# Optimization experiments

Hardware: AMD Instinct MI355X
Metric: run time of the kernel (lower is better)

## Reference

```python
import jax, jax.numpy as jnp
import numpy as np

N, E, G = 10000, 40000, 128          # nodes, edges, graphs
NF, EF, H, NH, GD, L = 92, 50, 64, 10, 108, 5  # feat dims, hidden, heads, global dim, layers
EPS = 1e-5

def _lrelu(v):
    return jax.nn.leaky_relu(v, 0.2)

def setup_inputs() -> dict:
    key = jax.random.key(0)
    ks = jax.random.split(key, 24)
    def rn(k, shp, s=0.05):
        return jax.random.normal(k, shp, jnp.float32) * s
    return {
        "x": jax.random.normal(ks[0], (N, NF), jnp.float32),
        "edge_index": jax.random.randint(ks[1], (2, E), 0, N, dtype=jnp.int32),
        "edge_attr": jax.random.normal(ks[2], (E, EF), jnp.float32),
        "batch_idx": jnp.sort(jax.random.randint(ks[3], (N,), 0, G, dtype=jnp.int32)),
        "global_features": jax.random.normal(ks[4], (G, GD), jnp.float32),
        "node_W": rn(ks[5], (NF, H)), "node_b": jnp.zeros((H,), jnp.float32),
        "edge_W": rn(ks[6], (EF, H)), "edge_b": jnp.zeros((H,), jnp.float32),
        "conv_W": rn(ks[7], (L, 2 * H, NH * H)),
        "conv_att": rn(ks[8], (L, NH, 2 * H)),
        "conv_b": jnp.zeros((L, H), jnp.float32),
        "conv_gamma": jnp.ones((L, NH), jnp.float32),
        "conv_beta": jnp.zeros((L, NH), jnp.float32),
        "ga_W1": rn(ks[9], (H + GD, H)), "ga_b1": jnp.zeros((H,), jnp.float32),
        "ga_W2": rn(ks[10], (H, 1)), "ga_b2": jnp.zeros((1,), jnp.float32),
        "out_W1": rn(ks[11], (H, H)), "out_b1": jnp.zeros((H,), jnp.float32),
        "out_W2": rn(ks[12], (H, 1)), "out_b2": jnp.zeros((1,), jnp.float32),
    }

def reference(x, edge_index, edge_attr, batch_idx, global_features,
              node_W, node_b, edge_W, edge_b,
              conv_W, conv_att, conv_b, conv_gamma, conv_beta,
              ga_W1, ga_b1, ga_W2, ga_b2, out_W1, out_b1, out_W2, out_b2):
    row, col = edge_index[0], edge_index[1]
    # embeddings
    h = _lrelu(x @ node_W + node_b)            # [N, H]
    ea = _lrelu(edge_attr @ edge_W + edge_b)   # [E, H]
    initial = h
    inv_std = 1.0 / jnp.sqrt(1.0 + EPS)        # DiffGroupNorm eval: running mean=0, var=1
    for i in range(L):
        xi = jnp.concatenate([h[row], ea], axis=-1)               # [E, 2H]
        xj = jnp.concatenate([h[col], ea], axis=-1)
        hi = _lrelu(xi @ conv_W[i]).reshape(E, NH, H)             # [E, NH, H]
        hj = _lrelu(xj @ conv_W[i]).reshape(E, NH, H)
        alpha = jnp.sum(jnp.concatenate([hi, hj], -1) * conv_att[i][None], -1)  # [E, NH]
        alpha = _lrelu(alpha)
        alpha = alpha * inv_std * conv_gamma[i] + conv_beta[i]
        alpha = jax.nn.softmax(alpha, axis=1)                     # softmax over heads
        msg = (hj * alpha[..., None]).reshape(E, NH * H)
        agg = jax.ops.segment_sum(msg, row, num_segments=N).reshape(N, NH, H)
        h_new = agg.mean(axis=1) + conv_b[i]
        h = h + h_new if i > 0 else h_new
    h = h + initial
    # global attention: softmax over nodes within each graph
    g = global_features[batch_idx]                                 # [N, GD]
    s = _lrelu(jnp.concatenate([h, g], -1) @ ga_W1 + ga_b1)
    score = (s @ ga_W2 + ga_b2)[:, 0]                              # [N]
    smax = jax.ops.segment_max(score, batch_idx, num_segments=G)
    ex = jnp.exp(score - smax[batch_idx])
    denom = jax.ops.segment_sum(ex, batch_idx, num_segments=G)
    w = (ex / denom[batch_idx])[:, None]
    h = h * w
    pooled = jax.ops.segment_sum(h, batch_idx, num_segments=G)     # [G, H]
    out = jax.nn.relu(pooled @ out_W1 + out_b1) @ out_W2 + out_b2
    return out[:, 0]
```

## Files before the change

### kernel.cpp

```cpp
#include <hip/hip_runtime.h>

#define LRELU(v) ((v) > 0.f ? (v) : 0.2f * (v))

template <int CTRL, int RMASK>
__device__ __forceinline__ float dpp_add(float v) {
  int moved = __builtin_amdgcn_update_dpp(0, __builtin_bit_cast(int, v), CTRL,
                                          RMASK, 0xf, true);
  return v + __builtin_bit_cast(float, moved);
}
__device__ __forceinline__ float wave_sum(float v) {
  v = dpp_add<0x111, 0xf>(v);
  v = dpp_add<0x112, 0xf>(v);
  v = dpp_add<0x114, 0xf>(v);
  v = dpp_add<0x118, 0xf>(v);
  v = dpp_add<0x142, 0xa>(v);
  v = dpp_add<0x143, 0xc>(v);
  return __builtin_bit_cast(
      float, __builtin_amdgcn_readlane(__builtin_bit_cast(int, v), 63));
}

__global__ __launch_bounds__(256) void embed2_kernel(
    const float* __restrict__ x, const float* __restrict__ nW,
    const float* __restrict__ nb, float* __restrict__ h0, int N_,
    const float* __restrict__ eattr, const float* __restrict__ eW,
    const float* __restrict__ eb, float* __restrict__ ea, int E_,
    int nodeBlocks) {
  const int lane = threadIdx.x & 63;
  const float *X, *W, *b;
  float* out;
  int M, K, r;
  if ((int)blockIdx.x < nodeBlocks) {
    r = blockIdx.x * 4 + (threadIdx.x >> 6);
    X = x; W = nW; b = nb; out = h0; M = N_; K = 92;
  } else {
    r = (blockIdx.x - nodeBlocks) * 4 + (threadIdx.x >> 6);
    X = eattr; W = eW; b = eb; out = ea; M = E_; K = 50;
  }
  r = __builtin_amdgcn_readfirstlane(r);
  if (r >= M) return;
  float acc = b[lane];
  const float* Xr = X + (size_t)r * K;
  const float* Wl = W + lane;
  for (int k = 0; k < K; ++k) acc = fmaf(Xr[k], Wl[(size_t)k * 64], acc);
  acc = LRELU(acc);
  out[(size_t)r * 64 + lane] = acc;
}

__global__ __launch_bounds__(256, 4) void update_gemm_kernel(
    const float* __restrict__ A0, float* __restrict__ h,
    float* __restrict__ agg, const float* __restrict__ bvec,
    const float* __restrict__ W, float* __restrict__ P, int M, int mode) {
  const int lane = threadIdx.x & 63;
  const int wv =
      __builtin_amdgcn_readfirstlane(blockIdx.x * 4 + (threadIdx.x >> 6));
  const int r0 = wv * 4;
  if (r0 >= M) return;
  float hv[4];
  if (mode < 0) {
#pragma unroll
    for (int r = 0; r < 4; ++r) hv[r] = A0[(size_t)(r0 + r) * 64 + lane];
  } else {
    float bl = bvec[lane];
#pragma unroll
    for (int r = 0; r < 4; ++r) {
      size_t idx = (size_t)(r0 + r) * 64 + lane;
      float v = fmaf(agg[idx], 0.1f, bl);
      if (mode >= 1) v += h[idx];
      agg[idx] = 0.f;
      h[idx] = v;
      hv[r] = v;
    }
  }
  float acc[4][10];
#pragma unroll
  for (int r = 0; r < 4; ++r)
#pragma unroll
    for (int q = 0; q < 10; ++q) acc[r][q] = 0.f;
  const float* Wl = W + lane;
  float wa[10], wb[10];
#pragma unroll
  for (int q = 0; q < 10; ++q) wa[q] = Wl[q * 64];
#pragma unroll 1
  for (int k = 0; k < 64; k += 2) {
#pragma unroll
    for (int q = 0; q < 10; ++q) wb[q] = Wl[(k + 1) * 640 + q * 64];
#pragma unroll
    for (int r = 0; r < 4; ++r) {
      float a = __shfl(hv[r], k);
#pragma unroll
      for (int q = 0; q < 10; ++q) acc[r][q] = fmaf(a, wa[q], acc[r][q]);
    }
    if (k + 2 < 64) {
#pragma unroll
      for (int q = 0; q < 10; ++q) wa[q] = Wl[(k + 2) * 640 + q * 64];
    }
#pragma unroll
    for (int r = 0; r < 4; ++r) {
      float a = __shfl(hv[r], k + 1);
#pragma unroll
      for (int q = 0; q < 10; ++q) acc[r][q] = fmaf(a, wb[q], acc[r][q]);
    }
  }
#pragma unroll
  for (int r = 0; r < 4; ++r) {
    float* Crow = P + (size_t)(r0 + r) * 640;
#pragma unroll
    for (int q = 0; q < 10; ++q) Crow[q * 64 + lane] = acc[r][q];
  }
}

__global__ __launch_bounds__(256, 3) void edge_fused_kernel(
    const float* __restrict__ P, const float* __restrict__ ea,
    const float* __restrict__ Wbot,
    const int* __restrict__ row, const int* __restrict__ col,
    const float* __restrict__ att, const float* __restrict__ gamma,
    const float* __restrict__ beta, float* __restrict__ agg, int E_) {
  const int lane = threadIdx.x & 63;
  const int wv =
      __builtin_amdgcn_readfirstlane(blockIdx.x * 4 + (threadIdx.x >> 6));
  const int e0 = wv * 8;
  if (e0 >= E_) return;

  int eix[8], ris[8], cis[8];
#pragma unroll
  for (int r = 0; r < 8; ++r) {
    int e = (e0 + r < E_) ? (e0 + r) : (E_ - 1);
    eix[r] = e;
    ris[r] = row[e];
    cis[r] = col[e];
  }

  float qacc[8][10];
#pragma unroll
  for (int r = 0; r < 8; ++r)
#pragma unroll
    for (int q = 0; q < 10; ++q) qacc[r][q] = 0.f;

  const float* Wl = Wbot + lane;
  float wa[10], wb[10];
#pragma unroll
  for (int q = 0; q < 10; ++q) wa[q] = Wl[q * 64];
#pragma unroll 1
  for (int k = 0; k < 64; k += 2) {
#pragma unroll
    for (int q = 0; q < 10; ++q) wb[q] = Wl[(k + 1) * 640 + q * 64];
#pragma unroll
    for (int r = 0; r < 8; ++r) {
      float a = ea[(size_t)eix[r] * 64 + k];
#pragma unroll
      for (int q = 0; q < 10; ++q) qacc[r][q] = fmaf(a, wa[q], qacc[r][q]);
    }
    if (k + 2 < 64) {
#pragma unroll
      for (int q = 0; q < 10; ++q) wa[q] = Wl[(k + 2) * 640 + q * 64];
    }
#pragma unroll
    for (int r = 0; r < 8; ++r) {
      float a = ea[(size_t)eix[r] * 64 + k + 1];
#pragma unroll
      for (int q = 0; q < 10; ++q) qacc[r][q] = fmaf(a, wb[q], qacc[r][q]);
    }
  }

  const float inv_std = 0.9999950000374997f;
  float gm[10], bt[10];
#pragma unroll
  for (int q = 0; q < 10; ++q) {
    gm[q] = gamma[q];
    bt[q] = beta[q];
  }

  float prb[10], pcb[10];
  {
    const float* Pr = P + (size_t)ris[0] * 640 + lane;
    const float* Pc = P + (size_t)cis[0] * 640 + lane;
#pragma unroll
    for (int q = 0; q < 10; ++q) {
      prb[q] = Pr[q * 64];
      pcb[q] = Pc[q * 64];
    }
  }

#pragma unroll
  for (int r = 0; r < 8; ++r) {
    if (e0 + r >= E_) break;
    float pr[10], pc[10];
#pragma unroll
    for (int q = 0; q < 10; ++q) {
      pr[q] = prb[q];
      pc[q] = pcb[q];
    }
    if (r + 1 < 8) {
      const float* Pr = P + (size_t)ris[r + 1] * 640 + lane;
      const float* Pc = P + (size_t)cis[r + 1] * 640 + lane;
#pragma unroll
      for (int q = 0; q < 10; ++q) {
        prb[q] = Pr[q * 64];
        pcb[q] = Pc[q * 64];
      }
    }
    float hj[10], sv[10];
#pragma unroll
    for (int q = 0; q < 10; ++q) {
      float qc = qacc[r][q];
      float hi = pr[q] + qc;
      float hjv = pc[q] + qc;
      hi = LRELU(hi);
      hjv = LRELU(hjv);
      hj[q] = hjv;
      float part =
          fmaf(hi, att[q * 128 + lane], hjv * att[q * 128 + 64 + lane]);
      sv[q] = wave_sum(part);
    }
    float mx = -1e30f;
#pragma unroll
    for (int q = 0; q < 10; ++q) {
      float a = sv[q];
      a = LRELU(a);
      a = fmaf(a * inv_std, gm[q], bt[q]);
      sv[q] = a;
      mx = fmaxf(mx, a);
    }
    float ssum = 0.f;
#pragma unroll
    for (int q = 0; q < 10; ++q) {
      float ex = __expf(sv[q] - mx);
      sv[q] = ex;
      ssum += ex;
    }
    float inv = 1.0f / ssum;
    float m = 0.f;
#pragma unroll
    for (int q = 0; q < 10; ++q) m = fmaf(sv[q] * inv, hj[q], m);
    atomicAdd(agg + (size_t)ris[r] * 64 + lane, m);
  }
}

__global__ __launch_bounds__(256) void finalize_kernel(
    float* __restrict__ h, float* __restrict__ agg, const float* __restrict__ b,
    const float* __restrict__ h0, int total) {
  int idx = blockIdx.x * 256 + threadIdx.x;
  if (idx >= total) return;
  int f = idx & 63;
  float v = fmaf(agg[idx], 0.1f, b[f]);
  agg[idx] = 0.f;
  h[idx] = v + h[idx] + h0[idx];
}

__global__ __launch_bounds__(256) void score_kernel(
    const float* __restrict__ h, const int* __restrict__ batch,
    const float* __restrict__ gf, const float* __restrict__ W1,
    const float* __restrict__ b1, const float* __restrict__ W2,
    const float* __restrict__ b2, float* __restrict__ score, int N_) {
  const int lane = threadIdx.x & 63;
  const int n =
      __builtin_amdgcn_readfirstlane(blockIdx.x * 4 + (threadIdx.x >> 6));
  if (n >= N_) return;
  float acc = b1[lane];
  const float* hn = h + (size_t)n * 64;
  const float* W1l = W1 + lane;
#pragma unroll 8
  for (int k = 0; k < 64; ++k) acc = fmaf(hn[k], W1l[k * 64], acc);
  const int bn = batch[n];
  const float* g = gf + (size_t)bn * 108;
#pragma unroll 4
  for (int k = 0; k < 108; ++k) acc = fmaf(g[k], W1l[(64 + k) * 64], acc);
  acc = LRELU(acc);
  float v = wave_sum(acc * W2[lane]);
  if (lane == 0) score[n] = v + b2[0];
}

__global__ void bounds_kernel(const int* __restrict__ batch,
                              int* __restrict__ start, int N_, int G_) {
  int n = blockIdx.x * blockDim.x + threadIdx.x;
  if (n >= N_) return;
  int b = batch[n];
  int bp = (n == 0) ? -1 : batch[n - 1];
  for (int g = bp + 1; g <= b; ++g) start[g] = n;
  if (n == N_ - 1)
    for (int g = b + 1; g <= G_; ++g) start[g] = N_;
}

__global__ __launch_bounds__(256) void pool_out_kernel(
    const float* __restrict__ h, const float* __restrict__ score,
    const int* __restrict__ start, const float* __restrict__ W1,
    const float* __restrict__ b1, const float* __restrict__ W2,
    const float* __restrict__ b2, float* __restrict__ out) {
  int g = blockIdx.x;
  int s0 = start[g], s1 = start[g + 1];
  int tid = threadIdx.x;
  __shared__ float red[256];
  __shared__ float pool[64];
  __shared__ float sh_smax, sh_denom;
  float lm = -1e30f;
  for (int n = s0 + tid; n < s1; n += 256) lm = fmaxf(lm, score[n]);
  red[tid] = lm;
  __syncthreads();
  for (int off = 128; off; off >>= 1) {
    if (tid < off) red[tid] = fmaxf(red[tid], red[tid + off]);
    __syncthreads();
  }
  if (tid == 0) sh_smax = red[0];
  __syncthreads();
  float smax = sh_smax;
  __syncthreads();
  float ls = 0.f;
  for (int n = s0 + tid; n < s1; n += 256) ls += __expf(score[n] - smax);
  red[tid] = ls;
  __syncthreads();
  for (int off = 128; off; off >>= 1) {
    if (tid < off) red[tid] += red[tid + off];
    __syncthreads();
  }
  if (tid == 0) sh_denom = red[0];
  __syncthreads();
  float denom = sh_denom;
  float invd = denom > 0.f ? 1.0f / denom : 0.f;
  __syncthreads();
  int f = tid & 63, sub = tid >> 6;
  float acc = 0.f;
  for (int n = s0 + sub; n < s1; n += 4)
    acc = fmaf(__expf(score[n] - smax), h[(size_t)n * 64 + f], acc);
  red[tid] = acc;
  __syncthreads();
  if (tid < 64)
    pool[tid] =
        (red[tid] + red[tid + 64] + red[tid + 128] + red[tid + 192]) * invd;
  __syncthreads();
  if (tid < 64) {
    float a = b1[tid];
#pragma unroll 8
    for (int k = 0; k < 64; ++k) a = fmaf(pool[k], W1[k * 64 + tid], a);
    a = fmaxf(a, 0.f);
    red[tid] = a * W2[tid];
  }
  __syncthreads();
  if (tid == 0) {
    float s = 0.f;
    for (int k = 0; k < 64; ++k) s += red[k];
    out[g] = s + b2[0];
  }
}

extern "C" void kernel_launch(void* const* d_in, const int* in_sizes, int n_in,
                              void* d_out, int out_size, void* d_ws,
                              size_t ws_size, hipStream_t stream) {
  const float* x          = (const float*)d_in[0];
  const int*   edge_index = (const int*)d_in[1];
  const float* edge_attr  = (const float*)d_in[2];
  const int*   batch_idx  = (const int*)d_in[3];
  const float* gf         = (const float*)d_in[4];
  const float* node_W     = (const float*)d_in[5];
  const float* node_b     = (const float*)d_in[6];
  const float* edge_W     = (const float*)d_in[7];
  const float* edge_b     = (const float*)d_in[8];
  const float* conv_W     = (const float*)d_in[9];
  const float* conv_att   = (const float*)d_in[10];
  const float* conv_b     = (const float*)d_in[11];
  const float* conv_gamma = (const float*)d_in[12];
  const float* conv_beta  = (const float*)d_in[13];
  const float* ga_W1      = (const float*)d_in[14];
  const float* ga_b1      = (const float*)d_in[15];
  const float* ga_W2      = (const float*)d_in[16];
  const float* ga_b2      = (const float*)d_in[17];
  const float* out_W1     = (const float*)d_in[18];
  const float* out_b1     = (const float*)d_in[19];
  const float* out_W2     = (const float*)d_in[20];
  const float* out_b2     = (const float*)d_in[21];
  float* out = (float*)d_out;

  const int N = in_sizes[3];
  const int E = in_sizes[2] / 50;
  const int G = in_sizes[4] / 108;
  const int L = 5;

  float* ws = (float*)d_ws;
  float* h    = ws;  ws += (size_t)N * 64;
  float* h0   = ws;  ws += (size_t)N * 64;
  float* ea   = ws;  ws += (size_t)E * 64;
  float* P    = ws;  ws += (size_t)N * 640;
  float* agg  = ws;  ws += (size_t)N * 64;
  float* scr  = ws;  ws += N;
  int* gstart = (int*)ws;

  const int* row = edge_index;
  const int* col = edge_index + E;

  int nodeBlocks = (N + 3) / 4;
  int edgeBlocks = (E + 3) / 4;
  embed2_kernel<<<nodeBlocks + edgeBlocks, 256, 0, stream>>>(
      x, node_W, node_b, h0, N, edge_attr, edge_W, edge_b, ea, E, nodeBlocks);
  (void)hipMemsetAsync(agg, 0, (size_t)N * 64 * sizeof(float), stream);

  for (int i = 0; i < L; ++i) {
    const float* Wi = conv_W + (size_t)i * 128 * 640;
    if (i == 0) {
      update_gemm_kernel<<<(N / 4 + 3) / 4, 256, 0, stream>>>(
          h0, h, agg, nullptr, Wi, P, N, -1);
    } else {
      update_gemm_kernel<<<(N / 4 + 3) / 4, 256, 0, stream>>>(
          nullptr, h, agg, conv_b + (i - 1) * 64, Wi, P, N,
          (i - 1) == 0 ? 0 : 1);
    }
    int waves = (E + 7) / 8;
    edge_fused_kernel<<<(waves + 3) / 4, 256, 0, stream>>>(
        P, ea, Wi + 64 * 640, row, col, conv_att + (size_t)i * 1280,
        conv_gamma + i * 10, conv_beta + i * 10, agg, E);
  }
  finalize_kernel<<<(N * 64 + 255) / 256, 256, 0, stream>>>(
      h, agg, conv_b + (L - 1) * 64, h0, N * 64);

  score_kernel<<<(N + 3) / 4, 256, 0, stream>>>(h, batch_idx, gf, ga_W1, ga_b1,
                                                ga_W2, ga_b2, scr, N);
  bounds_kernel<<<(N + 255) / 256, 256, 0, stream>>>(batch_idx, gstart, N, G);
  pool_out_kernel<<<G, 256, 0, stream>>>(h, scr, gstart, out_W1, out_b1, out_W2,
                                         out_b2, out);
}
```

Measured before the change: 688.6 us.

## Repack conv weights lane-major and broadcast row values via readlane

Adds a repack kernel that reorders conv_W so each lane's 10 head columns sit next to each other. The GEMM and edge kernels can then load weights and P rows with float2 vector loads, and P is stored in the same interleaved layout. Edge-attribute and h rows are now loaded once per lane into registers and broadcast with readlane, replacing per-k scalar global loads and shuffles. The cost is an extra repack kernel launched on every call, extra workspace, and a P layout that all of its consumers must agree on.

```diff
diff --git a/kernel.cpp b/kernel.cpp
--- a/kernel.cpp
+++ b/kernel.cpp
@@ -1,6 +1,11 @@
 #include <hip/hip_runtime.h>
 
 #define LRELU(v) ((v) > 0.f ? (v) : 0.2f * (v))
+
+__device__ __forceinline__ float lane_bcast(float v, int k) {
+  return __builtin_bit_cast(
+      float, __builtin_amdgcn_readlane(__builtin_bit_cast(int, v), k));
+}
 
 template <int CTRL, int RMASK>
 __device__ __forceinline__ float dpp_add(float v) {
@@ -17,6 +22,18 @@
   v = dpp_add<0x143, 0xc>(v);
   return __builtin_bit_cast(
       float, __builtin_amdgcn_readlane(__builtin_bit_cast(int, v), 63));
+}
+
+__global__ __launch_bounds__(256) void repack_kernel(
+    const float* __restrict__ convW, float* __restrict__ Wrep) {
+  int idx = blockIdx.x * 256 + threadIdx.x;
+  if (idx >= 5 * 2 * 64 * 640) return;
+  int c = idx % 640;
+  int q = c >> 6, l = c & 63;
+  int rowg = idx / 640;
+  int i = rowg >> 7;
+  int row = rowg & 127;
+  Wrep[((size_t)(i * 2) * 64 + row) * 640 + l * 10 + q] = convW[idx];
 }
 
 __global__ __launch_bounds__(256) void embed2_kernel(
@@ -49,7 +66,7 @@
 __global__ __launch_bounds__(256, 4) void update_gemm_kernel(
     const float* __restrict__ A0, float* __restrict__ h,
     float* __restrict__ agg, const float* __restrict__ bvec,
-    const float* __restrict__ W, float* __restrict__ P, int M, int mode) {
+    const float* __restrict__ Wrep, float* __restrict__ P, int M, int mode) {
   const int lane = threadIdx.x & 63;
   const int wv =
       __builtin_amdgcn_readfirstlane(blockIdx.x * 4 + (threadIdx.x >> 6));
@@ -76,42 +93,46 @@
   for (int r = 0; r < 4; ++r)
 #pragma unroll
     for (int q = 0; q < 10; ++q) acc[r][q] = 0.f;
-  const float* Wl = W + lane;
+  const float* Wl = Wrep + lane * 10;
   float wa[10], wb[10];
 #pragma unroll
-  for (int q = 0; q < 10; ++q) wa[q] = Wl[q * 64];
+  for (int j = 0; j < 5; ++j)
+    *(float2*)&wa[2 * j] = *(const float2*)(Wl + 2 * j);
 #pragma unroll 1
   for (int k = 0; k < 64; k += 2) {
 #pragma unroll
-    for (int q = 0; q < 10; ++q) wb[q] = Wl[(k + 1) * 640 + q * 64];
+    for (int j = 0; j < 5; ++j)
+      *(float2*)&wb[2 * j] = *(const float2*)(Wl + (k + 1) * 640 + 2 * j);
 #pragma unroll
     for (int r = 0; r < 4; ++r) {
-      float a = __shfl(hv[r], k);
+      float a = lane_bcast(hv[r], k);
 #pragma unroll
       for (int q = 0; q < 10; ++q) acc[r][q] = fmaf(a, wa[q], acc[r][q]);
     }
     if (k + 2 < 64) {
 #pragma unroll
-      for (int q = 0; q < 10; ++q) wa[q] = Wl[(k + 2) * 640 + q * 64];
+      for (int j = 0; j < 5; ++j)
+        *(float2*)&wa[2 * j] = *(const float2*)(Wl + (k + 2) * 640 + 2 * j);
     }
 #pragma unroll
     for (int r = 0; r < 4; ++r) {
-      float a = __shfl(hv[r], k + 1);
+      float a = lane_bcast(hv[r], k + 1);
 #pragma unroll
       for (int q = 0; q < 10; ++q) acc[r][q] = fmaf(a, wb[q], acc[r][q]);
     }
   }
 #pragma unroll
   for (int r = 0; r < 4; ++r) {
-    float* Crow = P + (size_t)(r0 + r) * 640;
-#pragma unroll
-    for (int q = 0; q < 10; ++q) Crow[q * 64 + lane] = acc[r][q];
+    float* Prow = P + (size_t)(r0 + r) * 640 + lane * 10;
+#pragma unroll
+    for (int j = 0; j < 5; ++j)
+      *(float2*)(Prow + 2 * j) = make_float2(acc[r][2 * j], acc[r][2 * j + 1]);
   }
 }
 
 __global__ __launch_bounds__(256, 3) void edge_fused_kernel(
     const float* __restrict__ P, const float* __restrict__ ea,
-    const float* __restrict__ Wbot,
+    const float* __restrict__ Wrep,
     const int* __restrict__ row, const int* __restrict__ col,
     const float* __restrict__ att, const float* __restrict__ gamma,
     const float* __restrict__ beta, float* __restrict__ agg, int E_) {
@@ -121,13 +142,14 @@
   const int e0 = wv * 8;
   if (e0 >= E_) return;
 
-  int eix[8], ris[8], cis[8];
+  int ris[8], cis[8];
+  float eareg[8];
 #pragma unroll
   for (int r = 0; r < 8; ++r) {
     int e = (e0 + r < E_) ? (e0 + r) : (E_ - 1);
-    eix[r] = e;
     ris[r] = row[e];
     cis[r] = col[e];
+    eareg[r] = ea[(size_t)e * 64 + lane];
   }
 
   float qacc[8][10];
@@ -136,27 +158,30 @@
 #pragma unroll
     for (int q = 0; q < 10; ++q) qacc[r][q] = 0.f;
 
-  const float* Wl = Wbot + lane;
+  const float* Wl = Wrep + lane * 10;
   float wa[10], wb[10];
 #pragma unroll
-  for (int q = 0; q < 10; ++q) wa[q] = Wl[q * 64];
+  for (int j = 0; j < 5; ++j)
+    *(float2*)&wa[2 * j] = *(const float2*)(Wl + 2 * j);
 #pragma unroll 1
   for (int k = 0; k < 64; k += 2) {
 #pragma unroll
-    for (int q = 0; q < 10; ++q) wb[q] = Wl[(k + 1) * 640 + q * 64];
+    for (int j = 0; j < 5; ++j)
+      *(float2*)&wb[2 * j] = *(const float2*)(Wl + (k + 1) * 640 + 2 * j);
 #pragma unroll
     for (int r = 0; r < 8; ++r) {
-      float a = ea[(size_t)eix[r] * 64 + k];
+      float a = lane_bcast(eareg[r], k);
 #pragma unroll
       for (int q = 0; q < 10; ++q) qacc[r][q] = fmaf(a, wa[q], qacc[r][q]);
     }
     if (k + 2 < 64) {
 #pragma unroll
-      for (int q = 0; q < 10; ++q) wa[q] = Wl[(k + 2) * 640 + q * 64];
+      for (int j = 0; j < 5; ++j)
+        *(float2*)&wa[2 * j] = *(const float2*)(Wl + (k + 2) * 640 + 2 * j);
     }
 #pragma unroll
     for (int r = 0; r < 8; ++r) {
-      float a = ea[(size_t)eix[r] * 64 + k + 1];
+      float a = lane_bcast(eareg[r], k + 1);
 #pragma unroll
       for (int q = 0; q < 10; ++q) qacc[r][q] = fmaf(a, wb[q], qacc[r][q]);
     }
@@ -172,12 +197,12 @@
 
   float prb[10], pcb[10];
   {
-    const float* Pr = P + (size_t)ris[0] * 640 + lane;
-    const float* Pc = P + (size_t)cis[0] * 640 + lane;
-#pragma unroll
-    for (int q = 0; q < 10; ++q) {
-      prb[q] = Pr[q * 64];
-      pcb[q] = Pc[q * 64];
+    const float* Pr = P + (size_t)ris[0] * 640 + lane * 10;
+    const float* Pc = P + (size_t)cis[0] * 640 + lane * 10;
+#pragma unroll
+    for (int j = 0; j < 5; ++j) {
+      *(float2*)&prb[2 * j] = *(const float2*)(Pr + 2 * j);
+      *(float2*)&pcb[2 * j] = *(const float2*)(Pc + 2 * j);
     }
   }
 
@@ -191,12 +216,12 @@
       pc[q] = pcb[q];
     }
     if (r + 1 < 8) {
-      const float* Pr = P + (size_t)ris[r + 1] * 640 + lane;
-      const float* Pc = P + (size_t)cis[r + 1] * 640 + lane;
-#pragma unroll
-      for (int q = 0; q < 10; ++q) {
-        prb[q] = Pr[q * 64];
-        pcb[q] = Pc[q * 64];
+      const float* Pr = P + (size_t)ris[r + 1] * 640 + lane * 10;
+      const float* Pc = P + (size_t)cis[r + 1] * 640 + lane * 10;
+#pragma unroll
+      for (int j = 0; j < 5; ++j) {
+        *(float2*)&prb[2 * j] = *(const float2*)(Pr + 2 * j);
+        *(float2*)&pcb[2 * j] = *(const float2*)(Pc + 2 * j);
       }
     }
     float hj[10], sv[10];
@@ -257,10 +282,11 @@
       __builtin_amdgcn_readfirstlane(blockIdx.x * 4 + (threadIdx.x >> 6));
   if (n >= N_) return;
   float acc = b1[lane];
-  const float* hn = h + (size_t)n * 64;
   const float* W1l = W1 + lane;
+  float hreg = h[(size_t)n * 64 + lane];
 #pragma unroll 8
-  for (int k = 0; k < 64; ++k) acc = fmaf(hn[k], W1l[k * 64], acc);
+  for (int k = 0; k < 64; ++k)
+    acc = fmaf(lane_bcast(hreg, k), W1l[k * 64], acc);
   const int bn = batch[n];
   const float* g = gf + (size_t)bn * 108;
 #pragma unroll 4
@@ -381,11 +407,14 @@
   float* P    = ws;  ws += (size_t)N * 640;
   float* agg  = ws;  ws += (size_t)N * 64;
   float* scr  = ws;  ws += N;
-  int* gstart = (int*)ws;
+  int* gstart = (int*)ws;  ws += G + 8;
+  float* Wrep = ws;  ws += (size_t)L * 2 * 64 * 640;
 
   const int* row = edge_index;
   const int* col = edge_index + E;
 
+  repack_kernel<<<(5 * 2 * 64 * 640 + 255) / 256, 256, 0, stream>>>(conv_W,
+                                                                    Wrep);
   int nodeBlocks = (N + 3) / 4;
   int edgeBlocks = (E + 3) / 4;
   embed2_kernel<<<nodeBlocks + edgeBlocks, 256, 0, stream>>>(
@@ -393,18 +422,19 @@
   (void)hipMemsetAsync(agg, 0, (size_t)N * 64 * sizeof(float), stream);
 
   for (int i = 0; i < L; ++i) {
-    const float* Wi = conv_W + (size_t)i * 128 * 640;
+    const float* Wtop = Wrep + (size_t)(i * 2 + 0) * 64 * 640;
+    const float* Wbot = Wrep + (size_t)(i * 2 + 1) * 64 * 640;
     if (i == 0) {
       update_gemm_kernel<<<(N / 4 + 3) / 4, 256, 0, stream>>>(
-          h0, h, agg, nullptr, Wi, P, N, -1);
+          h0, h, agg, nullptr, Wtop, P, N, -1);
     } else {
       update_gemm_kernel<<<(N / 4 + 3) / 4, 256, 0, stream>>>(
-          nullptr, h, agg, conv_b + (i - 1) * 64, Wi, P, N,
+          nullptr, h, agg, conv_b + (i - 1) * 64, Wtop, P, N,
           (i - 1) == 0 ? 0 : 1);
     }
     int waves = (E + 7) / 8;
     edge_fused_kernel<<<(waves + 3) / 4, 256, 0, stream>>>(
-        P, ea, Wi + 64 * 640, row, col, conv_att + (size_t)i * 1280,
+        P, ea, Wbot, row, col, conv_att + (size_t)i * 1280,
         conv_gamma + i * 10, conv_beta + i * 10, agg, E);
   }
   finalize_kernel<<<(N * 64 + 255) / 256, 256, 0, stream>>>(
```

Result: slower. 802.4 us (+16.5%).

## Restructure edge kernel per-head with transposed edge features and online softmax

Applied to the files above, without the earlier changes.

Adds a transpose kernel that stores edge embeddings column-major, so each wave reads 8 contiguous edge values per k with scalar-friendly loads. The edge kernel now loops over heads one at a time, computing the head's edge projection, the attention logit and an online (running-max) softmax accumulation. This drops the 80-register qacc array so occupancy can rise to 4 waves per SIMD. In exchange it adds one transpose pass and extra exp calls per head. Weight loads are also refetched per head, and the head loop with its wave reductions runs serially.

```diff
diff --git a/kernel.cpp b/kernel.cpp
--- a/kernel.cpp
+++ b/kernel.cpp
@@ -46,6 +46,24 @@
   out[(size_t)r * 64 + lane] = acc;
 }
 
+__global__ __launch_bounds__(256) void transpose_kernel(
+    const float* __restrict__ ea, float* __restrict__ eaT, int E_) {
+  __shared__ float tile[64][65];
+  int e0 = blockIdx.x * 64;
+  int c = threadIdx.x & 63, rr = threadIdx.x >> 6;
+#pragma unroll
+  for (int i = 0; i < 16; ++i) {
+    int r = rr + i * 4;
+    if (e0 + r < E_) tile[r][c] = ea[(size_t)(e0 + r) * 64 + c];
+  }
+  __syncthreads();
+#pragma unroll
+  for (int i = 0; i < 16; ++i) {
+    int cc = rr + i * 4;
+    if (e0 + c < E_) eaT[(size_t)cc * E_ + e0 + c] = tile[c][cc];
+  }
+}
+
 __global__ __launch_bounds__(256, 4) void update_gemm_kernel(
     const float* __restrict__ A0, float* __restrict__ h,
     float* __restrict__ agg, const float* __restrict__ bvec,
@@ -109,8 +127,8 @@
   }
 }
 
-__global__ __launch_bounds__(256, 3) void edge_fused_kernel(
-    const float* __restrict__ P, const float* __restrict__ ea,
+__global__ __launch_bounds__(256, 4) void edge_fused_kernel(
+    const float* __restrict__ P, const float* __restrict__ eaT,
     const float* __restrict__ Wbot,
     const int* __restrict__ row, const int* __restrict__ col,
     const float* __restrict__ att, const float* __restrict__ gamma,
@@ -121,118 +139,79 @@
   const int e0 = wv * 8;
   if (e0 >= E_) return;
 
-  int eix[8], ris[8], cis[8];
+  int ris[8], cis[8];
 #pragma unroll
   for (int r = 0; r < 8; ++r) {
     int e = (e0 + r < E_) ? (e0 + r) : (E_ - 1);
-    eix[r] = e;
     ris[r] = row[e];
     cis[r] = col[e];
   }
 
-  float qacc[8][10];
-#pragma unroll
-  for (int r = 0; r < 8; ++r)
-#pragma unroll
-    for (int q = 0; q < 10; ++q) qacc[r][q] = 0.f;
+  const float inv_std = 0.9999950000374997f;
+  float m[8], mx[8], ss[8];
+#pragma unroll
+  for (int r = 0; r < 8; ++r) {
+    m[r] = 0.f;
+    mx[r] = -1e30f;
+    ss[r] = 0.f;
+  }
 
   const float* Wl = Wbot + lane;
-  float wa[10], wb[10];
-#pragma unroll
-  for (int q = 0; q < 10; ++q) wa[q] = Wl[q * 64];
 #pragma unroll 1
-  for (int k = 0; k < 64; k += 2) {
-#pragma unroll
-    for (int q = 0; q < 10; ++q) wb[q] = Wl[(k + 1) * 640 + q * 64];
+  for (int h = 0; h < 10; ++h) {
+    float pr[8], pc[8];
 #pragma unroll
     for (int r = 0; r < 8; ++r) {
-      float a = ea[(size_t)eix[r] * 64 + k];
-#pragma unroll
-      for (int q = 0; q < 10; ++q) qacc[r][q] = fmaf(a, wa[q], qacc[r][q]);
-    }
-    if (k + 2 < 64) {
-#pragma unroll
-      for (int q = 0; q < 10; ++q) wa[q] = Wl[(k + 2) * 640 + q * 64];
-    }
+      pr[r] = P[(size_t)ris[r] * 640 + h * 64 + lane];
+      pc[r] = P[(size_t)cis[r] * 640 + h * 64 + lane];
+    }
+    float at_i = att[h * 128 + lane];
+    float at_j = att[h * 128 + 64 + lane];
+    float gm = gamma[h], bt = beta[h];
+
+    float qa[8];
+#pragma unroll
+    for (int r = 0; r < 8; ++r) qa[r] = 0.f;
+    const float* Wh = Wl + h * 64;
+    float wa = Wh[0];
+#pragma unroll 1
+    for (int k = 0; k < 64; k += 2) {
+      float wb = Wh[(size_t)(k + 1) * 640];
+      const float* s0 = eaT + (size_t)k * E_ + e0;
+      const float* s1 = eaT + (size_t)(k + 1) * E_ + e0;
+#pragma unroll
+      for (int r = 0; r < 8; ++r) qa[r] = fmaf(s0[r], wa, qa[r]);
+      if (k + 2 < 64) wa = Wh[(size_t)(k + 2) * 640];
+#pragma unroll
+      for (int r = 0; r < 8; ++r) qa[r] = fmaf(s1[r], wb, qa[r]);
+    }
+
 #pragma unroll
     for (int r = 0; r < 8; ++r) {
-      float a = ea[(size_t)eix[r] * 64 + k + 1];
-#pragma unroll
-      for (int q = 0; q < 10; ++q) qacc[r][q] = fmaf(a, wb[q], qacc[r][q]);
-    }
-  }
-
-  const float inv_std = 0.9999950000374997f;
-  float gm[10], bt[10];
-#pragma unroll
-  for (int q = 0; q < 10; ++q) {
-    gm[q] = gamma[q];
-    bt[q] = beta[q];
-  }
-
-  float prb[10], pcb[10];
-  {
-    const float* Pr = P + (size_t)ris[0] * 640 + lane;
-    const float* Pc = P + (size_t)cis[0] * 640 + lane;
-#pragma unroll
-    for (int q = 0; q < 10; ++q) {
-      prb[q] = Pr[q * 64];
-      pcb[q] = Pc[q * 64];
+      if (e0 + r < E_) {
+        float hi = pr[r] + qa[r];
+        float hjv = pc[r] + qa[r];
+        hi = LRELU(hi);
+        hjv = LRELU(hjv);
+        float part = fmaf(hi, at_i, hjv * at_j);
+        float s = wave_sum(part);
+        float a = LRELU(s);
+        a = fmaf(a * inv_std, gm, bt);
+        float nm = fmaxf(mx[r], a);
+        float scale = __expf(mx[r] - nm);
+        float ex = __expf(a - nm);
+        ss[r] = fmaf(ss[r], scale, ex);
+        m[r] = fmaf(m[r], scale, ex * hjv);
+        mx[r] = nm;
+      }
     }
   }
 
 #pragma unroll
   for (int r = 0; r < 8; ++r) {
     if (e0 + r >= E_) break;
-    float pr[10], pc[10];
-#pragma unroll
-    for (int q = 0; q < 10; ++q) {
-      pr[q] = prb[q];
-      pc[q] = pcb[q];
-    }
-    if (r + 1 < 8) {
-      const float* Pr = P + (size_t)ris[r + 1] * 640 + lane;
-      const float* Pc = P + (size_t)cis[r + 1] * 640 + lane;
-#pragma unroll
-      for (int q = 0; q < 10; ++q) {
-        prb[q] = Pr[q * 64];
-        pcb[q] = Pc[q * 64];
-      }
-    }
-    float hj[10], sv[10];
-#pragma unroll
-    for (int q = 0; q < 10; ++q) {
-      float qc = qacc[r][q];
-      float hi = pr[q] + qc;
-      float hjv = pc[q] + qc;
-      hi = LRELU(hi);
-      hjv = LRELU(hjv);
-      hj[q] = hjv;
-      float part =
-          fmaf(hi, att[q * 128 + lane], hjv * att[q * 128 + 64 + lane]);
-      sv[q] = wave_sum(part);
-    }
-    float mx = -1e30f;
-#pragma unroll
-    for (int q = 0; q < 10; ++q) {
-      float a = sv[q];
-      a = LRELU(a);
-      a = fmaf(a * inv_std, gm[q], bt[q]);
-      sv[q] = a;
-      mx = fmaxf(mx, a);
-    }
-    float ssum = 0.f;
-#pragma unroll
-    for (int q = 0; q < 10; ++q) {
-      float ex = __expf(sv[q] - mx);
-      sv[q] = ex;
-      ssum += ex;
-    }
-    float inv = 1.0f / ssum;
-    float m = 0.f;
-#pragma unroll
-    for (int q = 0; q < 10; ++q) m = fmaf(sv[q] * inv, hj[q], m);
-    atomicAdd(agg + (size_t)ris[r] * 64 + lane, m);
+    float inv = 1.0f / ss[r];
+    atomicAdd(agg + (size_t)ris[r] * 64 + lane, m[r] * inv);
   }
 }
 
@@ -378,6 +357,7 @@
   float* h    = ws;  ws += (size_t)N * 64;
   float* h0   = ws;  ws += (size_t)N * 64;
   float* ea   = ws;  ws += (size_t)E * 64;
+  float* eaT  = ws;  ws += (size_t)E * 64 + 16;
   float* P    = ws;  ws += (size_t)N * 640;
   float* agg  = ws;  ws += (size_t)N * 64;
   float* scr  = ws;  ws += N;
@@ -390,6 +370,7 @@
   int edgeBlocks = (E + 3) / 4;
   embed2_kernel<<<nodeBlocks + edgeBlocks, 256, 0, stream>>>(
       x, node_W, node_b, h0, N, edge_attr, edge_W, edge_b, ea, E, nodeBlocks);
+  transpose_kernel<<<(E + 63) / 64, 256, 0, stream>>>(ea, eaT, E);
   (void)hipMemsetAsync(agg, 0, (size_t)N * 64 * sizeof(float), stream);
 
   for (int i = 0; i < L; ++i) {
@@ -404,7 +385,7 @@
     }
     int waves = (E + 7) / 8;
     edge_fused_kernel<<<(waves + 3) / 4, 256, 0, stream>>>(
-        P, ea, Wi + 64 * 640, row, col, conv_att + (size_t)i * 1280,
+        P, eaT, Wi + 64 * 640, row, col, conv_att + (size_t)i * 1280,
         conv_gamma + i * 10, conv_beta + i * 10, agg, E);
   }
   finalize_kernel<<<(N * 64 + 255) / 256, 256, 0, stream>>>(
```

Measured after the change: 969.1 us. 40.7% more time.

## Sort edges by destination row and coalesce per-row atomic accumulation

Applied to the files above, without the earlier changes.

Adds a counting sort of edges by row (count, single-block scan, atomic scatter) and gathers edge embeddings into the sorted order once before the layer loop. The edge kernel then reads contiguous edge features and sorted row/col indices, and merges consecutive edges with the same row into a single atomicAdd per run. This targets scattered edge-feature loads and atomic contention on the aggregation buffer. It costs several extra small kernels, an extra E×64 buffer, and a serial single-block scan, and the scatter order within a row is nondeterministic, so the float summation order can vary between runs.

```diff
diff --git a/kernel.cpp b/kernel.cpp
--- a/kernel.cpp
+++ b/kernel.cpp
@@ -46,6 +46,59 @@
   out[(size_t)r * 64 + lane] = acc;
 }
 
+__global__ __launch_bounds__(256) void count_kernel(const int* __restrict__ row,
+                                                    int* __restrict__ cnt,
+                                                    int E_) {
+  int e = blockIdx.x * 256 + threadIdx.x;
+  if (e < E_) atomicAdd(&cnt[row[e]], 1);
+}
+
+__global__ __launch_bounds__(256) void scan_kernel(const int* __restrict__ cnt,
+                                                   int* __restrict__ cursor,
+                                                   int N_) {
+  __shared__ int part[256];
+  int t = threadIdx.x;
+  int per = (N_ + 255) / 256;
+  int lo = t * per, hi = min(N_, lo + per);
+  int s = 0;
+  for (int i = lo; i < hi; ++i) s += cnt[i];
+  part[t] = s;
+  __syncthreads();
+  for (int off = 1; off < 256; off <<= 1) {
+    int v = (t >= off) ? part[t - off] : 0;
+    __syncthreads();
+    part[t] += v;
+    __syncthreads();
+  }
+  int excl = (t == 0) ? 0 : part[t - 1];
+  for (int i = lo; i < hi; ++i) {
+    cursor[i] = excl;
+    excl += cnt[i];
+  }
+}
+
+__global__ __launch_bounds__(256) void scatter_kernel(
+    const int* __restrict__ row, const int* __restrict__ col,
+    int* __restrict__ cursor, int* __restrict__ rs, int* __restrict__ cs,
+    int* __restrict__ es, int E_) {
+  int e = blockIdx.x * 256 + threadIdx.x;
+  if (e >= E_) return;
+  int r = row[e];
+  int p = atomicAdd(&cursor[r], 1);
+  rs[p] = r;
+  cs[p] = col[e];
+  es[p] = e;
+}
+
+__global__ __launch_bounds__(256) void gather_ea_kernel(
+    const float* __restrict__ ea, const int* __restrict__ es,
+    float* __restrict__ eas, int E_) {
+  int idx = blockIdx.x * 256 + threadIdx.x;
+  if (idx >= E_ * 64) return;
+  int p = idx >> 6, c = idx & 63;
+  eas[idx] = ea[(size_t)es[p] * 64 + c];
+}
+
 __global__ __launch_bounds__(256, 4) void update_gemm_kernel(
     const float* __restrict__ A0, float* __restrict__ h,
     float* __restrict__ agg, const float* __restrict__ bvec,
@@ -110,9 +163,9 @@
 }
 
 __global__ __launch_bounds__(256, 3) void edge_fused_kernel(
-    const float* __restrict__ P, const float* __restrict__ ea,
+    const float* __restrict__ P, const float* __restrict__ eas,
     const float* __restrict__ Wbot,
-    const int* __restrict__ row, const int* __restrict__ col,
+    const int* __restrict__ rs, const int* __restrict__ cs,
     const float* __restrict__ att, const float* __restrict__ gamma,
     const float* __restrict__ beta, float* __restrict__ agg, int E_) {
   const int lane = threadIdx.x & 63;
@@ -121,13 +174,12 @@
   const int e0 = wv * 8;
   if (e0 >= E_) return;
 
-  int eix[8], ris[8], cis[8];
+  int ris[8], cis[8];
 #pragma unroll
   for (int r = 0; r < 8; ++r) {
     int e = (e0 + r < E_) ? (e0 + r) : (E_ - 1);
-    eix[r] = e;
-    ris[r] = row[e];
-    cis[r] = col[e];
+    ris[r] = rs[e];
+    cis[r] = cs[e];
   }
 
   float qacc[8][10];
@@ -136,6 +188,7 @@
 #pragma unroll
     for (int q = 0; q < 10; ++q) qacc[r][q] = 0.f;
 
+  const float* eaw = eas + (size_t)e0 * 64;
   const float* Wl = Wbot + lane;
   float wa[10], wb[10];
 #pragma unroll
@@ -146,7 +199,7 @@
     for (int q = 0; q < 10; ++q) wb[q] = Wl[(k + 1) * 640 + q * 64];
 #pragma unroll
     for (int r = 0; r < 8; ++r) {
-      float a = ea[(size_t)eix[r] * 64 + k];
+      float a = eaw[r * 64 + k];
 #pragma unroll
       for (int q = 0; q < 10; ++q) qacc[r][q] = fmaf(a, wa[q], qacc[r][q]);
     }
@@ -156,7 +209,7 @@
     }
 #pragma unroll
     for (int r = 0; r < 8; ++r) {
-      float a = ea[(size_t)eix[r] * 64 + k + 1];
+      float a = eaw[r * 64 + k + 1];
 #pragma unroll
       for (int q = 0; q < 10; ++q) qacc[r][q] = fmaf(a, wb[q], qacc[r][q]);
     }
@@ -180,6 +233,9 @@
       pcb[q] = Pc[q * 64];
     }
   }
+
+  float pend = 0.f;
+  int prow = ris[0];
 
 #pragma unroll
   for (int r = 0; r < 8; ++r) {
@@ -232,8 +288,14 @@
     float m = 0.f;
 #pragma unroll
     for (int q = 0; q < 10; ++q) m = fmaf(sv[q] * inv, hj[q], m);
-    atomicAdd(agg + (size_t)ris[r] * 64 + lane, m);
-  }
+    if (ris[r] != prow) {
+      atomicAdd(agg + (size_t)prow * 64 + lane, pend);
+      pend = 0.f;
+      prow = ris[r];
+    }
+    pend += m;
+  }
+  atomicAdd(agg + (size_t)prow * 64 + lane, pend);
 }
 
 __global__ __launch_bounds__(256) void finalize_kernel(
@@ -378,10 +440,16 @@
   float* h    = ws;  ws += (size_t)N * 64;
   float* h0   = ws;  ws += (size_t)N * 64;
   float* ea   = ws;  ws += (size_t)E * 64;
+  float* eas  = ws;  ws += (size_t)E * 64;
   float* P    = ws;  ws += (size_t)N * 640;
   float* agg  = ws;  ws += (size_t)N * 64;
   float* scr  = ws;  ws += N;
-  int* gstart = (int*)ws;
+  int* gstart = (int*)ws;  ws += G + 8;
+  int* cnt    = (int*)ws;  ws += N;
+  int* cursor = (int*)ws;  ws += N;
+  int* rs     = (int*)ws;  ws += E;
+  int* cs     = (int*)ws;  ws += E;
+  int* es     = (int*)ws;  ws += E;
 
   const int* row = edge_index;
   const int* col = edge_index + E;
@@ -390,6 +458,13 @@
   int edgeBlocks = (E + 3) / 4;
   embed2_kernel<<<nodeBlocks + edgeBlocks, 256, 0, stream>>>(
       x, node_W, node_b, h0, N, edge_attr, edge_W, edge_b, ea, E, nodeBlocks);
+
+  (void)hipMemsetAsync(cnt, 0, (size_t)N * sizeof(int), stream);
+  count_kernel<<<(E + 255) / 256, 256, 0, stream>>>(row, cnt, E);
+  scan_kernel<<<1, 256, 0, stream>>>(cnt, cursor, N);
+  scatter_kernel<<<(E + 255) / 256, 256, 0, stream>>>(row, col, cursor, rs, cs,
+                                                      es, E);
+  gather_ea_kernel<<<(E * 64 + 255) / 256, 256, 0, stream>>>(ea, es, eas, E);
   (void)hipMemsetAsync(agg, 0, (size_t)N * 64 * sizeof(float), stream);
 
   for (int i = 0; i < L; ++i) {
@@ -404,7 +479,7 @@
     }
     int waves = (E + 7) / 8;
     edge_fused_kernel<<<(waves + 3) / 4, 256, 0, stream>>>(
-        P, ea, Wi + 64 * 640, row, col, conv_att + (size_t)i * 1280,
+        P, eas, Wi + 64 * 640, rs, cs, conv_att + (size_t)i * 1280,
         conv_gamma + i * 10, conv_beta + i * 10, agg, E);
   }
   finalize_kernel<<<(N * 64 + 255) / 256, 256, 0, stream>>>(
```

Result: slower. 728.4 us (+5.8%).
